# Kernel optimization log

Hardware: AMD Instinct MI355X
Metric: run time of the kernel (lower is better)

## Reference

```python
import jax, jax.numpy as jnp
import numpy as np

N, E, F, H, G, U, A = 50000, 800000, 96, 96, 64, 32, 16


def _linear_params(key, fan_in, fan_out):
    # torch nn.Linear default init: U(-1/sqrt(fan_in), 1/sqrt(fan_in))
    s = 1.0 / np.sqrt(fan_in)
    kw, kb = jax.random.split(key)
    W = jax.random.uniform(kw, (fan_in, fan_out), jnp.float32, -s, s)
    b = jax.random.uniform(kb, (fan_out,), jnp.float32, -s, s)
    return W, b


def setup_inputs() -> dict:
    key = jax.random.key(0)
    ks = jax.random.split(key, 12)
    x = jax.random.normal(ks[0], (N, F), jnp.float32)
    edge_index = jax.random.randint(ks[1], (2, E), 0, N, dtype=jnp.int32)
    batch = jnp.sort(jax.random.randint(ks[2], (N,), 0, G, dtype=jnp.int32))
    u = jax.random.normal(ks[3], (G, U), jnp.float32)
    W1, b1 = _linear_params(ks[4], F, H)      # conv1
    W2, b2 = _linear_params(ks[5], H, H)      # conv2
    aW1, ab1 = _linear_params(ks[6], H + U, H)
    aW2, ab2 = _linear_params(ks[7], H, A)
    cW1, cb1 = _linear_params(ks[8], H + U, H)
    cW2, cb2 = _linear_params(ks[9], H, 1)
    return {"x": x, "edge_index": edge_index, "batch": batch, "u": u,
            "W1": W1, "b1": b1, "W2": W2, "b2": b2,
            "aW1": aW1, "ab1": ab1, "aW2": aW2, "ab2": ab2,
            "cW1": cW1, "cb1": cb1, "cW2": cW2, "cb2": cb2}


def reference(x, edge_index, batch, u, W1, b1, W2, b2,
              aW1, ab1, aW2, ab2, cW1, cb1, cW2, cb2):
    n = x.shape[0]
    src, dst = edge_index[0], edge_index[1]
    # GCN symmetric normalization with self-loops (PyG GCNConv defaults)
    deg = jnp.zeros((n,), x.dtype).at[dst].add(1.0) + 1.0  # +1 for self-loop
    dis = jax.lax.rsqrt(deg)                               # deg^{-1/2}
    edge_norm = (dis[src] * dis[dst])[:, None]             # [E,1]
    self_norm = (dis * dis)[:, None]                       # [N,1] = deg^{-1}

    def gcn(h, W, b):
        h = h @ W                                          # linear (bias after agg)
        agg = jax.ops.segment_sum(h[src] * edge_norm, dst, num_segments=n)
        return agg + h * self_norm + b

    h = jax.nn.relu(gcn(x, W1, b1))
    h = jax.nn.relu(gcn(h, W2, b2))

    # global mean pool over graphs
    cnt = jax.ops.segment_sum(jnp.ones((n,), h.dtype), batch, num_segments=G)
    pooled = jax.ops.segment_sum(h, batch, num_segments=G) / jnp.maximum(cnt, 1.0)[:, None]

    comb = jnp.concatenate([pooled, u], axis=1)            # [G, H+U]
    action_logits = jax.nn.relu(comb @ aW1 + ab1) @ aW2 + ab2   # [G, A]
    state_value = jax.nn.relu(comb @ cW1 + cb1) @ cW2 + cb2     # [G, 1]
    return action_logits, state_value
```

## Files before the change

### kernel.cpp

```cpp
#include <hip/hip_runtime.h>
#include <hip/hip_bf16.h>

#define FH 96
#define GU 32
#define GA 16
#define NG 64

typedef __attribute__((ext_vector_type(8))) short bf16x8;
typedef __attribute__((ext_vector_type(8))) unsigned short u16x8;
typedef __attribute__((ext_vector_type(4))) float f32x4;

static __device__ __forceinline__ unsigned short f2bf(float f) {
    unsigned int u = __float_as_uint(f);
    unsigned int r = (u + 0x7fffu + ((u >> 16) & 1u)) >> 16;
    return (unsigned short)r;
}
static __device__ __forceinline__ float bf2f(unsigned short h) {
    return __uint_as_float(((unsigned int)h) << 16);
}

__global__ void zero_k(float4* __restrict__ p, int n4) {
    int i = blockIdx.x * blockDim.x + threadIdx.x;
    if (i < n4) p[i] = make_float4(0.f, 0.f, 0.f, 0.f);
}

__global__ void count_deg_k(const int* __restrict__ dst, int* __restrict__ deg,
                            unsigned short* __restrict__ rank16, int E) {
    int e = blockIdx.x * blockDim.x + threadIdx.x;
    if (e < E) rank16[e] = (unsigned short)atomicAdd(&deg[dst[e]], 1);
}

__global__ __launch_bounds__(256) void partial_k(const int* __restrict__ deg,
                                                 int* __restrict__ blockSums, int n) {
    int base = blockIdx.x * 1024;
    int t = threadIdx.x;
    int s = 0;
#pragma unroll
    for (int j = 0; j < 4; j++) {
        int i = base + t * 4 + j;
        if (i < n) s += deg[i];
    }
    __shared__ int red[4];
    for (int off = 32; off > 0; off >>= 1) s += __shfl_down(s, off, 64);
    if ((t & 63) == 0) red[t >> 6] = s;
    __syncthreads();
    if (t == 0) blockSums[blockIdx.x] = red[0] + red[1] + red[2] + red[3];
}

__global__ __launch_bounds__(256) void scanpart_k(const int* __restrict__ blockSums,
                                                  int* __restrict__ blockOff, int nb) {
    __shared__ int sh[256];
    int t = threadIdx.x;
    sh[t] = (t < nb) ? blockSums[t] : 0;
    __syncthreads();
    for (int off = 1; off < 256; off <<= 1) {
        int v = 0;
        if (t >= off) v = sh[t - off];
        __syncthreads();
        if (t >= off) sh[t] += v;
        __syncthreads();
    }
    if (t < nb) blockOff[t] = (t == 0) ? 0 : sh[t - 1];
}

__global__ __launch_bounds__(256) void emit_k(const int* __restrict__ deg,
                                              const int* __restrict__ blockOff,
                                              int* __restrict__ rowstart,
                                              float* __restrict__ dis, int n) {
    __shared__ int sh[256];
    int base = blockIdx.x * 1024;
    int t = threadIdx.x;
    int d[4];
    int s = 0;
#pragma unroll
    for (int j = 0; j < 4; j++) {
        int i = base + t * 4 + j;
        d[j] = (i < n) ? deg[i] : 0;
        s += d[j];
    }
    sh[t] = s;
    __syncthreads();
    for (int off = 1; off < 256; off <<= 1) {
        int v = 0;
        if (t >= off) v = sh[t - off];
        __syncthreads();
        if (t >= off) sh[t] += v;
        __syncthreads();
    }
    int run = blockOff[blockIdx.x] + ((t == 0) ? 0 : sh[t - 1]);
#pragma unroll
    for (int j = 0; j < 4; j++) {
        int i = base + t * 4 + j;
        if (i < n) {
            rowstart[i] = run;
            dis[i] = rsqrtf((float)d[j] + 1.0f);
        }
        run += d[j];
    }
    if (blockIdx.x == gridDim.x - 1 && t == 255) rowstart[n] = run;
}

__global__ void fill_k(const int* __restrict__ src, const int* __restrict__ dst,
                       const int* __restrict__ rowstart,
                       const unsigned short* __restrict__ rank16,
                       unsigned short* __restrict__ csr, int E) {
    int e = blockIdx.x * blockDim.x + threadIdx.x;
    if (e < E) {
        int pos = rowstart[dst[e]] + (int)rank16[e];
        csr[pos] = (unsigned short)src[e];
    }
}

__global__ __launch_bounds__(256) void convW_k(const float* __restrict__ W1,
                                               const float* __restrict__ W2,
                                               unsigned short* __restrict__ WB1,
                                               unsigned short* __restrict__ WB2) {
    const float* W = (blockIdx.x == 0) ? W1 : W2;
    unsigned short* WB = (blockIdx.x == 0) ? WB1 : WB2;
    for (int idx = threadIdx.x; idx < 2 * 3 * 6 * 64 * 8; idx += 256) {
        int j = idx & 7;
        int lane = (idx >> 3) & 63;
        int frag = idx >> 9;
        int cg = frag % 6;
        int rest = frag / 6;
        int ks = rest % 3;
        int t = rest / 3;
        int k = ks * 32 + (lane >> 4) * 8 + j;
        int n = cg * 16 + (lane & 15);
        float w = W[k * FH + n];
        unsigned short h = f2bf(w);
        WB[idx] = (t == 0) ? h : f2bf(w - bf2f(h));
    }
}

template <int INMODE>
__global__ __launch_bounds__(256, 3) void gemm_mfma_k(
    const float* __restrict__ Xf,
    const unsigned short* __restrict__ Xh, const unsigned short* __restrict__ Xl,
    const unsigned short* __restrict__ WB, const float* __restrict__ scale,
    unsigned short* __restrict__ Yb, int nrows) {
    int lane = threadIdx.x & 63;
    int wid  = threadIdx.x >> 6;
    int wr = wid >> 1, wc = wid & 1;
    int row0 = blockIdx.x * 64 + wr * 32;

    bf16x8 b[2][3][3];
#pragma unroll
    for (int t = 0; t < 2; t++)
#pragma unroll
        for (int ks = 0; ks < 3; ks++)
#pragma unroll
            for (int cg = 0; cg < 3; cg++) {
                int frag = (t * 3 + ks) * 6 + wc * 3 + cg;
                b[t][ks][cg] = *(const bf16x8*)(WB + frag * 512 + lane * 8);
            }

    f32x4 acc[2][3];
#pragma unroll
    for (int rg = 0; rg < 2; rg++)
#pragma unroll
        for (int cg = 0; cg < 3; cg++) acc[rg][cg] = (f32x4){0.f, 0.f, 0.f, 0.f};

    int r0 = lane & 15;
    int kcol = (lane >> 4) * 8;
#pragma unroll
    for (int ks = 0; ks < 3; ks++) {
        bf16x8 ah[2], al[2];
#pragma unroll
        for (int rg = 0; rg < 2; rg++) {
            if (INMODE == 1) {
                size_t off = (size_t)(row0 + rg * 16 + r0) * FH + ks * 32 + kcol;
                ah[rg] = *(const bf16x8*)(Xh + off);
                al[rg] = *(const bf16x8*)(Xl + off);
            } else {
                int rr = row0 + rg * 16 + r0;
                if (rr >= nrows) rr = nrows - 1;
                const float* xp = Xf + (size_t)rr * FH + ks * 32 + kcol;
                float4 v0 = *(const float4*)xp;
                float4 v1 = *(const float4*)(xp + 4);
                float xv[8] = {v0.x, v0.y, v0.z, v0.w, v1.x, v1.y, v1.z, v1.w};
                bf16x8 hh, ll;
#pragma unroll
                for (int j = 0; j < 8; j++) {
                    unsigned short h = f2bf(xv[j]);
                    hh[j] = (short)h;
                    ll[j] = (short)f2bf(xv[j] - bf2f(h));
                }
                ah[rg] = hh;
                al[rg] = ll;
            }
        }
#pragma unroll
        for (int rg = 0; rg < 2; rg++)
#pragma unroll
            for (int cg = 0; cg < 3; cg++)
                acc[rg][cg] = __builtin_amdgcn_mfma_f32_16x16x32_bf16(
                    ah[rg], b[0][ks][cg], acc[rg][cg], 0, 0, 0);
#pragma unroll
        for (int rg = 0; rg < 2; rg++)
#pragma unroll
            for (int cg = 0; cg < 3; cg++)
                acc[rg][cg] = __builtin_amdgcn_mfma_f32_16x16x32_bf16(
                    ah[rg], b[1][ks][cg], acc[rg][cg], 0, 0, 0);
#pragma unroll
        for (int rg = 0; rg < 2; rg++)
#pragma unroll
            for (int cg = 0; cg < 3; cg++)
                acc[rg][cg] = __builtin_amdgcn_mfma_f32_16x16x32_bf16(
                    al[rg], b[0][ks][cg], acc[rg][cg], 0, 0, 0);
    }

#pragma unroll
    for (int rg = 0; rg < 2; rg++) {
#pragma unroll
        for (int r = 0; r < 4; r++) {
            int row = row0 + rg * 16 + (lane >> 4) * 4 + r;
            if (row < nrows) {
                float s = scale[row];
#pragma unroll
                for (int cg = 0; cg < 3; cg++) {
                    int col = wc * 48 + cg * 16 + (lane & 15);
                    Yb[(size_t)row * FH + col] = f2bf(acc[rg][cg][r] * s);
                }
            }
        }
    }
}

static __device__ __forceinline__ void gather_core(
    const unsigned short* __restrict__ hXb, const float* __restrict__ dis,
    const int* __restrict__ rowstart, const unsigned short* __restrict__ csr,
    const float* __restrict__ bias, int node, int f8, float o[8]) {
    int s = rowstart[node];
    int e = rowstart[node + 1];
    u16x8 sv = *(const u16x8*)&hXb[node * FH + f8];
    float a[8];
#pragma unroll
    for (int j = 0; j < 8; j++) a[j] = bf2f((unsigned short)sv[j]);
    int p = s;
    for (; p + 4 <= e; p += 4) {
        int i0 = csr[p], i1 = csr[p + 1], i2 = csr[p + 2], i3 = csr[p + 3];
        u16x8 v0 = *(const u16x8*)&hXb[i0 * FH + f8];
        u16x8 v1 = *(const u16x8*)&hXb[i1 * FH + f8];
        u16x8 v2 = *(const u16x8*)&hXb[i2 * FH + f8];
        u16x8 v3 = *(const u16x8*)&hXb[i3 * FH + f8];
#pragma unroll
        for (int j = 0; j < 8; j++) {
            a[j] += (bf2f((unsigned short)v0[j]) + bf2f((unsigned short)v1[j]))
                  + (bf2f((unsigned short)v2[j]) + bf2f((unsigned short)v3[j]));
        }
    }
    for (; p < e; p++) {
        int i0 = csr[p];
        u16x8 v0 = *(const u16x8*)&hXb[i0 * FH + f8];
#pragma unroll
        for (int j = 0; j < 8; j++) a[j] += bf2f((unsigned short)v0[j]);
    }
    float dn = dis[node];
    float4 bv0 = *(const float4*)&bias[f8];
    float4 bv1 = *(const float4*)&bias[f8 + 4];
    float bb[8] = {bv0.x, bv0.y, bv0.z, bv0.w, bv1.x, bv1.y, bv1.z, bv1.w};
#pragma unroll
    for (int j = 0; j < 8; j++) o[j] = fmaxf(a[j] * dn + bb[j], 0.0f);
}

__global__ __launch_bounds__(256) void gather12a_k(
    const unsigned short* __restrict__ hXb, const float* __restrict__ dis,
    const int* __restrict__ rowstart, const unsigned short* __restrict__ csr,
    const float* __restrict__ bias, unsigned short* __restrict__ outH,
    unsigned short* __restrict__ outL, int n) {
    int idx = blockIdx.x * blockDim.x + threadIdx.x;
    if (idx >= n * 12) return;
    int node = idx / 12;
    int f8 = (idx - node * 12) * 8;
    float o[8];
    gather_core(hXb, dis, rowstart, csr, bias, node, f8, o);
    u16x8 hh, ll;
#pragma unroll
    for (int j = 0; j < 8; j++) {
        unsigned short h = f2bf(o[j]);
        hh[j] = h;
        ll[j] = f2bf(o[j] - bf2f(h));
    }
    *(u16x8*)&outH[node * FH + f8] = hh;
    *(u16x8*)&outL[node * FH + f8] = ll;
}

__global__ __launch_bounds__(256) void gather12p_k(
    const unsigned short* __restrict__ hXb, const float* __restrict__ dis,
    const int* __restrict__ rowstart, const unsigned short* __restrict__ csr,
    const float* __restrict__ bias, const int* __restrict__ batch,
    float* __restrict__ pooled, float* __restrict__ cnt, int n) {
    __shared__ float lp[NG * FH];
    __shared__ float lc[NG];
    for (int i = threadIdx.x; i < NG * FH; i += 256) lp[i] = 0.0f;
    if (threadIdx.x < NG) lc[threadIdx.x] = 0.0f;
    __syncthreads();

    int idx = blockIdx.x * blockDim.x + threadIdx.x;
    bool active = (idx < n * 12);
    int node = 0, f8 = 0, fq = 0;
    if (active) {
        node = idx / 12;
        fq = idx - node * 12;
        f8 = fq * 8;
        float o[8];
        gather_core(hXb, dis, rowstart, csr, bias, node, f8, o);
        int g = batch[node];
#pragma unroll
        for (int j = 0; j < 8; j++) atomicAdd(&lp[g * FH + f8 + j], o[j]);
        if (fq == 0) atomicAdd(&lc[g], 1.0f);
    }
    __syncthreads();
    for (int i = threadIdx.x; i < NG * FH; i += 256)
        if (lp[i] != 0.0f) atomicAdd(&pooled[i], lp[i]);
    if (threadIdx.x < NG)
        if (lc[threadIdx.x] != 0.0f) atomicAdd(&cnt[threadIdx.x], lc[threadIdx.x]);
}

__global__ __launch_bounds__(128) void head_k(const float* __restrict__ pooled,
                                              const float* __restrict__ cnt,
                                              const float* __restrict__ u,
                                              const float* __restrict__ aW1, const float* __restrict__ ab1,
                                              const float* __restrict__ aW2, const float* __restrict__ ab2,
                                              const float* __restrict__ cW1, const float* __restrict__ cb1,
                                              const float* __restrict__ cW2, const float* __restrict__ cb2,
                                              float* __restrict__ out, int G) {
    int g = blockIdx.x;
    int t = threadIdx.x;
    __shared__ float comb[FH + GU];
    __shared__ float hidA[FH];
    __shared__ float hidC[FH];
    __shared__ float tmp[FH];
    float c = fmaxf(cnt[g], 1.0f);
    if (t < FH) comb[t] = pooled[g * FH + t] / c;
    else if (t < FH + GU) comb[t] = u[g * GU + (t - FH)];
    __syncthreads();
    if (t < FH) {
        float a = ab1[t], cc = cb1[t];
        for (int k = 0; k < FH + GU; k++) {
            float cv = comb[k];
            a += cv * aW1[k * FH + t];
            cc += cv * cW1[k * FH + t];
        }
        hidA[t] = fmaxf(a, 0.0f);
        hidC[t] = fmaxf(cc, 0.0f);
    }
    __syncthreads();
    if (t < GA) {
        float a = ab2[t];
        for (int j = 0; j < FH; j++) a += hidA[j] * aW2[j * GA + t];
        out[g * GA + t] = a;
    }
    if (t >= 32 && t < 32 + FH) tmp[t - 32] = hidC[t - 32] * cW2[t - 32];
    __syncthreads();
    if (t == 0) {
        float v = cb2[0];
        for (int j = 0; j < FH; j++) v += tmp[j];
        out[G * GA + g] = v;
    }
}

extern "C" void kernel_launch(void* const* d_in, const int* in_sizes, int n_in,
                              void* d_out, int out_size, void* d_ws, size_t ws_size,
                              hipStream_t stream) {
    const float* x   = (const float*)d_in[0];
    const int*   ei  = (const int*)d_in[1];
    const int*   bat = (const int*)d_in[2];
    const float* u   = (const float*)d_in[3];
    const float* W1  = (const float*)d_in[4];
    const float* b1  = (const float*)d_in[5];
    const float* W2  = (const float*)d_in[6];
    const float* b2  = (const float*)d_in[7];
    const float* aW1 = (const float*)d_in[8];
    const float* ab1 = (const float*)d_in[9];
    const float* aW2 = (const float*)d_in[10];
    const float* ab2 = (const float*)d_in[11];
    const float* cW1 = (const float*)d_in[12];
    const float* cb1 = (const float*)d_in[13];
    const float* cW2 = (const float*)d_in[14];
    const float* cb2 = (const float*)d_in[15];
    float* out = (float*)d_out;

    const int N = in_sizes[0] / FH;
    const int E = in_sizes[1] / 2;
    const int G = in_sizes[3] / GU;
    const int NPAD = (N + 63) / 64 * 64;

    const int* src = ei;
    const int* dst = ei + E;

    float* ws = (float*)d_ws;
    size_t o = 0;
    int*   degI     = (int*)(ws + o);   o += NPAD;
    float* pooled   = ws + o;           o += NG * FH;
    float* cnt      = ws + o;           o += 64;
    size_t zero_elems = o;
    float* dis      = ws + o;           o += NPAD;
    int*   rowstart = (int*)(ws + o);   o += NPAD;
    int*   blockSums= (int*)(ws + o);   o += 512;
    int*   blockOff = (int*)(ws + o);   o += 512;
    unsigned short* rank16 = (unsigned short*)(ws + o); o += ((size_t)(E + 1) / 2 + 63) / 64 * 64;
    unsigned short* csr16  = (unsigned short*)(ws + o); o += ((size_t)(E + 1) / 2 + 63) / 64 * 64;
    unsigned short* WB1 = (unsigned short*)(ws + o); o += 9216;
    unsigned short* WB2 = (unsigned short*)(ws + o); o += 9216;
    unsigned short* Xh = (unsigned short*)(ws + o);
    unsigned short* Xl = Xh + (size_t)NPAD * FH;
    o += (size_t)NPAD * FH;
    unsigned short* hXb = (unsigned short*)(ws + o); o += (size_t)NPAD * FH / 2;
    (void)ws_size;

    int gridE = (E + 255) / 256;
    int gridG12 = (N * 12 + 255) / 256;
    int gridMfma = NPAD / 64;
    int nbScan = (N + 1023) / 1024;
    int n4zero = (int)(zero_elems / 4);
    int gridZero = (n4zero + 255) / 256;

    zero_k<<<gridZero, 256, 0, stream>>>((float4*)ws, n4zero);

    count_deg_k<<<gridE, 256, 0, stream>>>(dst, degI, rank16, E);
    partial_k<<<nbScan, 256, 0, stream>>>(degI, blockSums, N);
    scanpart_k<<<1, 256, 0, stream>>>(blockSums, blockOff, nbScan);
    emit_k<<<nbScan, 256, 0, stream>>>(degI, blockOff, rowstart, dis, N);
    fill_k<<<gridE, 256, 0, stream>>>(src, dst, rowstart, rank16, csr16, E);

    convW_k<<<2, 256, 0, stream>>>(W1, W2, WB1, WB2);

    gemm_mfma_k<0><<<gridMfma, 256, 0, stream>>>(x, (const unsigned short*)nullptr,
                                                 (const unsigned short*)nullptr,
                                                 WB1, dis, hXb, N);
    gather12a_k<<<gridG12, 256, 0, stream>>>(hXb, dis, rowstart, csr16, b1, Xh, Xl, N);
    gemm_mfma_k<1><<<gridMfma, 256, 0, stream>>>((const float*)nullptr, Xh, Xl,
                                                 WB2, dis, hXb, N);
    gather12p_k<<<gridG12, 256, 0, stream>>>(hXb, dis, rowstart, csr16, b2,
                                             bat, pooled, cnt, N);

    head_k<<<G, 128, 0, stream>>>(pooled, cnt, u, aW1, ab1, aW2, ab2,
                                  cW1, cb1, cW2, cb2, out, G);
}
```

Baseline: 200.7 us.

## Drop low-part bf16 split for layer-2 input and split pooling into separate kernel

The first-layer output is now stored as a single bf16 array instead of a hi/lo split pair. The second GEMM therefore runs two MFMA passes per k-step instead of three and reads half the input bytes. The pooling fused into the second gather, which used a per-block 24KB shared-memory accumulator and shared atomics, is replaced by a plain gather that writes bf16 output plus a separate pool kernel that walks the sorted batch in node chunks. This lowers accuracy of the layer-2 input and adds an extra kernel launch and an extra bf16 write/read of the hidden state.

```diff
diff --git a/kernel.cpp b/kernel.cpp
--- a/kernel.cpp
+++ b/kernel.cpp
@@ -135,8 +135,7 @@
 
 template <int INMODE>
 __global__ __launch_bounds__(256, 3) void gemm_mfma_k(
-    const float* __restrict__ Xf,
-    const unsigned short* __restrict__ Xh, const unsigned short* __restrict__ Xl,
+    const float* __restrict__ Xf, const unsigned short* __restrict__ Xb,
     const unsigned short* __restrict__ WB, const float* __restrict__ scale,
     unsigned short* __restrict__ Yb, int nrows) {
     int lane = threadIdx.x & 63;
@@ -170,8 +169,7 @@
         for (int rg = 0; rg < 2; rg++) {
             if (INMODE == 1) {
                 size_t off = (size_t)(row0 + rg * 16 + r0) * FH + ks * 32 + kcol;
-                ah[rg] = *(const bf16x8*)(Xh + off);
-                al[rg] = *(const bf16x8*)(Xl + off);
+                ah[rg] = *(const bf16x8*)(Xb + off);
             } else {
                 int rr = row0 + rg * 16 + r0;
                 if (rr >= nrows) rr = nrows - 1;
@@ -202,12 +200,14 @@
             for (int cg = 0; cg < 3; cg++)
                 acc[rg][cg] = __builtin_amdgcn_mfma_f32_16x16x32_bf16(
                     ah[rg], b[1][ks][cg], acc[rg][cg], 0, 0, 0);
-#pragma unroll
-        for (int rg = 0; rg < 2; rg++)
-#pragma unroll
-            for (int cg = 0; cg < 3; cg++)
-                acc[rg][cg] = __builtin_amdgcn_mfma_f32_16x16x32_bf16(
-                    al[rg], b[0][ks][cg], acc[rg][cg], 0, 0, 0);
+        if (INMODE == 0) {
+#pragma unroll
+            for (int rg = 0; rg < 2; rg++)
+#pragma unroll
+                for (int cg = 0; cg < 3; cg++)
+                    acc[rg][cg] = __builtin_amdgcn_mfma_f32_16x16x32_bf16(
+                        al[rg], b[0][ks][cg], acc[rg][cg], 0, 0, 0);
+        }
     }
 
 #pragma unroll
@@ -227,10 +227,14 @@
     }
 }
 
-static __device__ __forceinline__ void gather_core(
+__global__ __launch_bounds__(256) void gather12_k(
     const unsigned short* __restrict__ hXb, const float* __restrict__ dis,
     const int* __restrict__ rowstart, const unsigned short* __restrict__ csr,
-    const float* __restrict__ bias, int node, int f8, float o[8]) {
+    const float* __restrict__ bias, unsigned short* __restrict__ outB, int n) {
+    int idx = blockIdx.x * blockDim.x + threadIdx.x;
+    if (idx >= n * 12) return;
+    int node = idx / 12;
+    int f8 = (idx - node * 12) * 8;
     int s = rowstart[node];
     int e = rowstart[node + 1];
     u16x8 sv = *(const u16x8*)&hXb[node * FH + f8];
@@ -260,62 +264,40 @@
     float4 bv0 = *(const float4*)&bias[f8];
     float4 bv1 = *(const float4*)&bias[f8 + 4];
     float bb[8] = {bv0.x, bv0.y, bv0.z, bv0.w, bv1.x, bv1.y, bv1.z, bv1.w};
-#pragma unroll
-    for (int j = 0; j < 8; j++) o[j] = fmaxf(a[j] * dn + bb[j], 0.0f);
-}
-
-__global__ __launch_bounds__(256) void gather12a_k(
-    const unsigned short* __restrict__ hXb, const float* __restrict__ dis,
-    const int* __restrict__ rowstart, const unsigned short* __restrict__ csr,
-    const float* __restrict__ bias, unsigned short* __restrict__ outH,
-    unsigned short* __restrict__ outL, int n) {
-    int idx = blockIdx.x * blockDim.x + threadIdx.x;
-    if (idx >= n * 12) return;
-    int node = idx / 12;
-    int f8 = (idx - node * 12) * 8;
-    float o[8];
-    gather_core(hXb, dis, rowstart, csr, bias, node, f8, o);
-    u16x8 hh, ll;
-#pragma unroll
-    for (int j = 0; j < 8; j++) {
-        unsigned short h = f2bf(o[j]);
-        hh[j] = h;
-        ll[j] = f2bf(o[j] - bf2f(h));
-    }
-    *(u16x8*)&outH[node * FH + f8] = hh;
-    *(u16x8*)&outL[node * FH + f8] = ll;
-}
-
-__global__ __launch_bounds__(256) void gather12p_k(
-    const unsigned short* __restrict__ hXb, const float* __restrict__ dis,
-    const int* __restrict__ rowstart, const unsigned short* __restrict__ csr,
-    const float* __restrict__ bias, const int* __restrict__ batch,
-    float* __restrict__ pooled, float* __restrict__ cnt, int n) {
-    __shared__ float lp[NG * FH];
-    __shared__ float lc[NG];
-    for (int i = threadIdx.x; i < NG * FH; i += 256) lp[i] = 0.0f;
-    if (threadIdx.x < NG) lc[threadIdx.x] = 0.0f;
-    __syncthreads();
-
-    int idx = blockIdx.x * blockDim.x + threadIdx.x;
-    bool active = (idx < n * 12);
-    int node = 0, f8 = 0, fq = 0;
-    if (active) {
-        node = idx / 12;
-        fq = idx - node * 12;
-        f8 = fq * 8;
-        float o[8];
-        gather_core(hXb, dis, rowstart, csr, bias, node, f8, o);
-        int g = batch[node];
-#pragma unroll
-        for (int j = 0; j < 8; j++) atomicAdd(&lp[g * FH + f8 + j], o[j]);
-        if (fq == 0) atomicAdd(&lc[g], 1.0f);
-    }
-    __syncthreads();
-    for (int i = threadIdx.x; i < NG * FH; i += 256)
-        if (lp[i] != 0.0f) atomicAdd(&pooled[i], lp[i]);
-    if (threadIdx.x < NG)
-        if (lc[threadIdx.x] != 0.0f) atomicAdd(&cnt[threadIdx.x], lc[threadIdx.x]);
+    u16x8 hh;
+#pragma unroll
+    for (int j = 0; j < 8; j++) hh[j] = f2bf(fmaxf(a[j] * dn + bb[j], 0.0f));
+    *(u16x8*)&outB[node * FH + f8] = hh;
+}
+
+__global__ __launch_bounds__(128) void pool2_k(const unsigned short* __restrict__ h,
+                                               const int* __restrict__ bat,
+                                               float* __restrict__ pooled,
+                                               float* __restrict__ cnt, int n) {
+    const int CH = 256;
+    int beg = blockIdx.x * CH;
+    if (beg >= n) return;
+    int end = min(beg + CH, n);
+    int t = threadIdx.x;
+    if (t < FH) {
+        float acc = 0.f;
+        int g = bat[beg];
+        for (int node = beg; node < end; ++node) {
+            int gg = bat[node];
+            if (gg != g) { atomicAdd(&pooled[g * FH + t], acc); acc = 0.f; g = gg; }
+            acc += bf2f(h[(size_t)node * FH + t]);
+        }
+        atomicAdd(&pooled[g * FH + t], acc);
+    } else if (t == FH) {
+        float c = 0.f;
+        int g = bat[beg];
+        for (int node = beg; node < end; ++node) {
+            int gg = bat[node];
+            if (gg != g) { atomicAdd(&cnt[g], c); c = 0.f; g = gg; }
+            c += 1.f;
+        }
+        atomicAdd(&cnt[g], c);
+    }
 }
 
 __global__ __launch_bounds__(128) void head_k(const float* __restrict__ pooled,
@@ -404,16 +386,17 @@
     unsigned short* csr16  = (unsigned short*)(ws + o); o += ((size_t)(E + 1) / 2 + 63) / 64 * 64;
     unsigned short* WB1 = (unsigned short*)(ws + o); o += 9216;
     unsigned short* WB2 = (unsigned short*)(ws + o); o += 9216;
-    unsigned short* Xh = (unsigned short*)(ws + o);
-    unsigned short* Xl = Xh + (size_t)NPAD * FH;
-    o += (size_t)NPAD * FH;
+    unsigned short* XhB = (unsigned short*)(ws + o); o += (size_t)NPAD * FH / 2;
     unsigned short* hXb = (unsigned short*)(ws + o); o += (size_t)NPAD * FH / 2;
     (void)ws_size;
+
+    unsigned short* h2b = XhB;
 
     int gridE = (E + 255) / 256;
     int gridG12 = (N * 12 + 255) / 256;
     int gridMfma = NPAD / 64;
     int nbScan = (N + 1023) / 1024;
+    int gridN = (N + 255) / 256;
     int n4zero = (int)(zero_elems / 4);
     int gridZero = (n4zero + 255) / 256;
 
@@ -428,14 +411,13 @@
     convW_k<<<2, 256, 0, stream>>>(W1, W2, WB1, WB2);
 
     gemm_mfma_k<0><<<gridMfma, 256, 0, stream>>>(x, (const unsigned short*)nullptr,
-                                                 (const unsigned short*)nullptr,
                                                  WB1, dis, hXb, N);
-    gather12a_k<<<gridG12, 256, 0, stream>>>(hXb, dis, rowstart, csr16, b1, Xh, Xl, N);
-    gemm_mfma_k<1><<<gridMfma, 256, 0, stream>>>((const float*)nullptr, Xh, Xl,
+    gather12_k<<<gridG12, 256, 0, stream>>>(hXb, dis, rowstart, csr16, b1, XhB, N);
+    gemm_mfma_k<1><<<gridMfma, 256, 0, stream>>>((const float*)nullptr, XhB,
                                                  WB2, dis, hXb, N);
-    gather12p_k<<<gridG12, 256, 0, stream>>>(hXb, dis, rowstart, csr16, b2,
-                                             bat, pooled, cnt, N);
-
+    gather12_k<<<gridG12, 256, 0, stream>>>(hXb, dis, rowstart, csr16, b2, h2b, N);
+
+    pool2_k<<<gridN, 128, 0, stream>>>(h2b, bat, pooled, cnt, N);
     head_k<<<G, 128, 0, stream>>>(pooled, cnt, u, aW1, ab1, aW2, ab2,
                                   cW1, cb1, cW2, cb2, out, G);
 }
```

Measured after the change: 235.4 us. 17.3% more time.
